# Kernel tuning notes

Hardware: AMD Instinct MI355X
Metric: run time of the kernel (lower is better)

## Reference

```python
import jax, jax.numpy as jnp
import numpy as np

B, D, H1, H2 = 512, 1024, 512, 128

def setup_inputs() -> dict:
    key = jax.random.key(0)
    ks = jax.random.split(key, 3)
    x = jax.random.normal(ks[0], (B, D), dtype=jnp.float32)
    W1 = jax.random.normal(ks[1], (H1, D), dtype=jnp.float32)
    W2 = jax.random.normal(ks[2], (H2, H1), dtype=jnp.float32)
    b1 = jnp.full((H1,), 0.1, dtype=jnp.float32)
    b2 = jnp.full((H2,), 0.1, dtype=jnp.float32)
    b3 = jnp.full((H1,), 0.1, dtype=jnp.float32)
    b_r = jnp.full((D,), 0.1, dtype=jnp.float32)
    return {"x": x, "W1": W1, "b1": b1, "W2": W2, "b2": b2, "b3": b3, "b_r": b_r}

def reference(x, W1, b1, W2, b2, b3, b_r):
    # encoder
    c1 = jax.nn.sigmoid(x @ W1.T + b1)          # [B, H1]
    c2 = jax.nn.sigmoid(c1 @ W2.T + b2)         # [B, H2]
    # decoder (tied weights)
    c3 = jax.nn.sigmoid(c2 @ W2 + b3)           # [B, H1]
    recover = c3 @ W1 + b_r                     # [B, D]
    # Jacobian of code w.r.t. x, batched (replaces per-sample diag+matmul loop):
    # Jac[b] = diag(c2'(b)) @ W2 @ diag(c1'(b)) @ W1
    s1p = c1 * (1.0 - c1)                       # [B, H1]
    s2p = c2 * (1.0 - c2)                       # [B, H2]
    M = s2p[:, :, None] * W2[None, :, :] * s1p[:, None, :]   # [B, H2, H1]
    Jac = jnp.einsum('bhk,kd->bhd', M, W1)      # [B, H2, D]
    return (recover, c2, Jac)
```

## Files before the change

kernel.cpp:

```cpp
#include <hip/hip_runtime.h>


typedef _Float16 f16x8 __attribute__((ext_vector_type(8)));
typedef _Float16 f16x4 __attribute__((ext_vector_type(4)));
typedef float    f32x4 __attribute__((ext_vector_type(4)));
typedef float    f32x2 __attribute__((ext_vector_type(2)));

__device__ __forceinline__ void gld_lds16(const _Float16* src, _Float16* dst_wave_uniform) {
    __builtin_amdgcn_global_load_lds((const __attribute__((address_space(1))) unsigned int*)src,
                                     (__attribute__((address_space(3))) unsigned int*)dst_wave_uniform,
                                     16, 0, 0);
}

__global__ __launch_bounds__(256) void prep_kernel(const float* __restrict__ W1,
                                                   const float* __restrict__ W2,
                                                   _Float16* __restrict__ W1T,
                                                   _Float16* __restrict__ W2h) {
    int bx = blockIdx.x;
    if (bx < 512) {
        __shared__ float tile[32][33];
        int dt = (bx & 31) * 32, kt = (bx >> 5) * 32;
        int tx = threadIdx.x & 31, ty = threadIdx.x >> 5;
        #pragma unroll
        for (int r = 0; r < 32; r += 8)
            tile[ty + r][tx] = W1[(kt + ty + r) * 1024 + dt + tx];
        __syncthreads();
        #pragma unroll
        for (int r = 0; r < 32; r += 8)
            W1T[(size_t)(dt + ty + r) * 512 + kt + tx] = (_Float16)tile[tx][ty + r];
    } else {
        int i = (bx - 512) * 1024 + threadIdx.x * 4;
        f32x4 v = *(const f32x4*)(W2 + i);
        f16x4 h;
        h.x = (_Float16)v.x; h.y = (_Float16)v.y; h.z = (_Float16)v.z; h.w = (_Float16)v.w;
        *(f16x4*)(W2h + i) = h;
    }
}

template <int EPI, bool TRANSB>
__global__ __launch_bounds__(256) void gemm_f32(const float* __restrict__ A,
                                                const float* __restrict__ Bm,
                                                const float* __restrict__ bias,
                                                float* __restrict__ C,
                                                float* __restrict__ Cd,
                                                _Float16* __restrict__ Ch,
                                                int M, int N, int K) {
    __shared__ __align__(16) float As[16][34];
    __shared__ __align__(16) float Bs[16][68];
    const int n0 = blockIdx.x * 64, m0 = blockIdx.y * 32;
    const int tid = threadIdx.x, tx = tid & 15, ty = tid >> 4;
    float acc[2][4] = {};

    for (int k0 = 0; k0 < K; k0 += 16) {
        #pragma unroll
        for (int r = 0; r < 2; ++r) {
            int m = (tid >> 4) + r * 16, k = tid & 15;
            As[k][m] = A[(size_t)(m0 + m) * K + k0 + k];
        }
        if (TRANSB) {
            #pragma unroll
            for (int r = 0; r < 4; ++r) {
                int n = (tid >> 4) + r * 16, k = tid & 15;
                Bs[k][n] = Bm[(size_t)(n0 + n) * K + k0 + k];
            }
        } else {
            #pragma unroll
            for (int r = 0; r < 4; ++r) {
                int k = (tid >> 6) + r * 4, n = tid & 63;
                Bs[k][n] = Bm[(size_t)(k0 + k) * N + n0 + n];
            }
        }
        __syncthreads();
        #pragma unroll
        for (int k = 0; k < 16; ++k) {
            f32x2 av = *(const f32x2*)&As[k][ty * 2];
            f32x4 bv = *(const f32x4*)&Bs[k][tx * 4];
            #pragma unroll
            for (int i = 0; i < 2; ++i)
                #pragma unroll
                for (int j = 0; j < 4; ++j)
                    acc[i][j] += av[i] * bv[j];
        }
        __syncthreads();
    }

    #pragma unroll
    for (int i = 0; i < 2; ++i) {
        int row = m0 + ty * 2 + i;
        #pragma unroll
        for (int j = 0; j < 4; ++j) {
            int col = n0 + tx * 4 + j;
            float z = acc[i][j] + bias[col];
            float s = 1.f / (1.f + __expf(-z));
            if constexpr (EPI == 1) {
                C[(size_t)row * N + col]  = s;
                Cd[(size_t)row * N + col] = s * (1.f - s);
            } else {
                Ch[(size_t)row * N + col] = (_Float16)s;
            }
        }
    }
}

__global__ __launch_bounds__(256) void build_A(const float* __restrict__ W2,
                                               const float* __restrict__ s1p,
                                               const float* __restrict__ s2p,
                                               _Float16* __restrict__ A_all) {
    const int b = blockIdx.x, tid = threadIdx.x;
    __shared__ float S1[512];
    __shared__ float S2[128];
    S1[tid]       = s1p[(size_t)b * 512 + tid];
    S1[tid + 256] = s1p[(size_t)b * 512 + tid + 256];
    if (tid < 128) S2[tid] = s2p[(size_t)b * 128 + tid];
    __syncthreads();
    _Float16* out = A_all + (size_t)b * 65536;
    #pragma unroll 4
    for (int i = 0; i < 32; ++i) {
        int c = tid + 256 * i;
        int h = c >> 6, k8 = (c & 63) * 8;
        f32x4 w0 = *(const f32x4*)(W2 + h * 512 + k8);
        f32x4 w1 = *(const f32x4*)(W2 + h * 512 + k8 + 4);
        float s2 = S2[h];
        f16x8 o;
        o[0] = (_Float16)(s2 * w0.x * S1[k8 + 0]);
        o[1] = (_Float16)(s2 * w0.y * S1[k8 + 1]);
        o[2] = (_Float16)(s2 * w0.z * S1[k8 + 2]);
        o[3] = (_Float16)(s2 * w0.w * S1[k8 + 3]);
        o[4] = (_Float16)(s2 * w1.x * S1[k8 + 4]);
        o[5] = (_Float16)(s2 * w1.y * S1[k8 + 5]);
        o[6] = (_Float16)(s2 * w1.z * S1[k8 + 6]);
        o[7] = (_Float16)(s2 * w1.w * S1[k8 + 7]);
        *(f16x8*)(out + h * 512 + k8) = o;
    }
}

template <bool HAS_BIAS>
__global__ __launch_bounds__(256) void mfma_bt(const _Float16* __restrict__ Abase,
                                               const _Float16* __restrict__ Bmat,
                                               const float* __restrict__ bias,
                                               float* __restrict__ OutBase,
                                               int K, int N,
                                               long aBatch, long oBatch) {
    __shared__ __align__(16) _Float16 Asl[128 * 64];
    __shared__ __align__(16) _Float16 Bsl[128 * 64];
    __shared__ float Bias[128];
    const _Float16* A = Abase + (size_t)blockIdx.z * aBatch;
    float* Out = OutBase + (size_t)blockIdx.z * oBatch;
    const int m0 = blockIdx.y * 128, n0 = blockIdx.x * 128;
    const int tid = threadIdx.x;
    const int lane = tid & 63, wave = tid >> 6;
    const int wm = (wave >> 1) * 64, wn = (wave & 1) * 64;
    const int l15 = lane & 15, q = lane >> 4;

    if (HAS_BIAS && tid < 128) Bias[tid] = bias[n0 + tid];

    f32x4 acc[4][4];
    #pragma unroll
    for (int i = 0; i < 4; ++i)
        #pragma unroll
        for (int j = 0; j < 4; ++j) acc[i][j] = (f32x4){0.f, 0.f, 0.f, 0.f};

    const int rbase = wave * 8 + (lane >> 3);
    const int kof   = (lane & 7) * 8;

    for (int k0 = 0; k0 < K; k0 += 64) {
        #pragma unroll
        for (int r = 0; r < 4; ++r) {
            gld_lds16(A    + (size_t)(m0 + r * 32 + rbase) * K + k0 + kof, Asl + (r * 32 + wave * 8) * 64);
            gld_lds16(Bmat + (size_t)(n0 + r * 32 + rbase) * K + k0 + kof, Bsl + (r * 32 + wave * 8) * 64);
        }
        __syncthreads();
        #pragma unroll
        for (int kk = 0; kk < 64; kk += 32) {
            f16x8 af[4], bf[4];
            #pragma unroll
            for (int i = 0; i < 4; ++i)
                af[i] = *(const f16x8*)(Asl + (wm + i * 16 + l15) * 64 + kk + q * 8);
            #pragma unroll
            for (int j = 0; j < 4; ++j)
                bf[j] = *(const f16x8*)(Bsl + (wn + j * 16 + l15) * 64 + kk + q * 8);
            #pragma unroll
            for (int i = 0; i < 4; ++i)
                #pragma unroll
                for (int j = 0; j < 4; ++j)
                    acc[i][j] = __builtin_amdgcn_mfma_f32_16x16x32_f16(af[i], bf[j], acc[i][j], 0, 0, 0);
        }
        __syncthreads();
    }

    #pragma unroll
    for (int i = 0; i < 4; ++i) {
        #pragma unroll
        for (int rg = 0; rg < 4; ++rg) {
            int m = m0 + wm + i * 16 + q * 4 + rg;
            #pragma unroll
            for (int j = 0; j < 4; ++j) {
                int dcol = wn + j * 16 + l15;
                float v = acc[i][j][rg];
                if (HAS_BIAS) v += Bias[dcol];
                Out[(size_t)m * N + n0 + dcol] = v;
            }
        }
    }
}

__global__ __launch_bounds__(256) void jac_kernel(const _Float16* __restrict__ W2h,
                                                  const _Float16* __restrict__ W1T,
                                                  const float* __restrict__ s1p,
                                                  const float* __restrict__ s2p,
                                                  float* __restrict__ Jac) {
    __shared__ __align__(16) _Float16 Asl[128 * 64];
    __shared__ __align__(16) _Float16 Bsl[128 * 64];
    __shared__ float Ssl[128];
    const int b  = blockIdx.y;
    const int n0 = blockIdx.x * 128;
    const int tid = threadIdx.x;
    const int lane = tid & 63, wave = tid >> 6;
    const int wm = (wave >> 1) * 64, wn = (wave & 1) * 64;
    const int l15 = lane & 15, q = lane >> 4;

    if (tid < 128) Ssl[tid] = s2p[b * 128 + tid];

    f32x4 acc[4][4];
    #pragma unroll
    for (int i = 0; i < 4; ++i)
        #pragma unroll
        for (int j = 0; j < 4; ++j) acc[i][j] = (f32x4){0.f, 0.f, 0.f, 0.f};

    const int ah  = tid >> 4;
    const int akq = (tid & 15) * 4;
    const int rbase = wave * 8 + (lane >> 3);
    const int kof   = (lane & 7) * 8;

    for (int k0 = 0; k0 < 512; k0 += 64) {
        f32x4 s4 = *(const f32x4*)(s1p + (size_t)b * 512 + k0 + akq);
        f16x4 s4h;
        s4h.x = (_Float16)s4.x; s4h.y = (_Float16)s4.y;
        s4h.z = (_Float16)s4.z; s4h.w = (_Float16)s4.w;
        #pragma unroll
        for (int r = 0; r < 8; ++r) {
            int h = ah + r * 16;
            f16x4 w4 = *(const f16x4*)(W2h + (size_t)h * 512 + k0 + akq);
            *(f16x4*)(Asl + h * 64 + akq) = w4 * s4h;
        }
        #pragma unroll
        for (int r = 0; r < 4; ++r)
            gld_lds16(W1T + (size_t)(n0 + r * 32 + rbase) * 512 + k0 + kof,
                      Bsl + (r * 32 + wave * 8) * 64);
        __syncthreads();

        #pragma unroll
        for (int kk = 0; kk < 64; kk += 32) {
            f16x8 af[4], bf[4];
            #pragma unroll
            for (int i = 0; i < 4; ++i)
                af[i] = *(const f16x8*)(Asl + (wm + i * 16 + l15) * 64 + kk + q * 8);
            #pragma unroll
            for (int j = 0; j < 4; ++j)
                bf[j] = *(const f16x8*)(Bsl + (wn + j * 16 + l15) * 64 + kk + q * 8);
            #pragma unroll
            for (int i = 0; i < 4; ++i)
                #pragma unroll
                for (int j = 0; j < 4; ++j)
                    acc[i][j] = __builtin_amdgcn_mfma_f32_16x16x32_f16(af[i], bf[j], acc[i][j], 0, 0, 0);
        }
        __syncthreads();
    }

    float* outb = Jac + (size_t)b * (128 * 1024);
    #pragma unroll
    for (int i = 0; i < 4; ++i) {
        #pragma unroll
        for (int rg = 0; rg < 4; ++rg) {
            int h = wm + i * 16 + q * 4 + rg;
            float s = Ssl[h];
            #pragma unroll
            for (int j = 0; j < 4; ++j) {
                int d = n0 + wn + j * 16 + l15;
                outb[(size_t)h * 1024 + d] = acc[i][j][rg] * s;
            }
        }
    }
}

extern "C" void kernel_launch(void* const* d_in, const int* in_sizes, int n_in,
                              void* d_out, int out_size, void* d_ws, size_t ws_size,
                              hipStream_t stream) {
    const float* x  = (const float*)d_in[0];
    const float* W1 = (const float*)d_in[1];
    const float* b1 = (const float*)d_in[2];
    const float* W2 = (const float*)d_in[3];
    const float* b2 = (const float*)d_in[4];
    const float* b3 = (const float*)d_in[5];
    const float* br = (const float*)d_in[6];

    float* out_rec = (float*)d_out;
    float* out_c2  = out_rec + 512 * 1024;
    float* out_jac = out_c2 + 512 * 128;

    char* ws = (char*)d_ws;
    _Float16* W1T   = (_Float16*)(ws);
    _Float16* W2h   = (_Float16*)(ws + 0x100000);
    float*    c1    = (float*)(ws + 0x120000);
    float*    s1p   = (float*)(ws + 0x220000);
    float*    s2p   = (float*)(ws + 0x320000);
    _Float16* c3h   = (_Float16*)(ws + 0x360000);
    _Float16* A_all = (_Float16*)(ws + 0x400000);
    const bool big_ws = ws_size >= (size_t)0x4400000;

    prep_kernel<<<576, 256, 0, stream>>>(W1, W2, W1T, W2h);
    gemm_f32<1, true ><<<dim3(8, 16), 256, 0, stream>>>(x,      W1, b1, c1,     s1p, nullptr, 512, 512, 1024);
    gemm_f32<1, true ><<<dim3(2, 16), 256, 0, stream>>>(c1,     W2, b2, out_c2, s2p, nullptr, 512, 128, 512);
    gemm_f32<2, false><<<dim3(8, 16), 256, 0, stream>>>(out_c2, W2, b3, nullptr, nullptr, c3h, 512, 512, 128);
    mfma_bt<true><<<dim3(8, 4, 1), 256, 0, stream>>>(c3h, W1T, br, out_rec, 512, 1024, 0, 0);
    if (big_ws) {
        build_A<<<512, 256, 0, stream>>>(W2, s1p, s2p, A_all);
        mfma_bt<false><<<dim3(8, 1, 512), 256, 0, stream>>>(A_all, W1T, nullptr, out_jac,
                                                            512, 1024, 65536, 131072);
    } else {
        jac_kernel<<<dim3(8, 512), 256, 0, stream>>>(W2h, W1T, s1p, s2p, out_jac);
    }
}
```

Baseline: 459.8 us.

## Fuse kernels, pipeline Jacobian GEMM with on-the-fly A build and double buffering

```diff
diff --git a/kernel.cpp b/kernel.cpp
--- a/kernel.cpp
+++ b/kernel.cpp
@@ -12,67 +12,70 @@
                                      16, 0, 0);
 }
 
-__global__ __launch_bounds__(256) void prep_kernel(const float* __restrict__ W1,
-                                                   const float* __restrict__ W2,
-                                                   _Float16* __restrict__ W1T,
-                                                   _Float16* __restrict__ W2h) {
-    int bx = blockIdx.x;
-    if (bx < 512) {
-        __shared__ float tile[32][33];
-        int dt = (bx & 31) * 32, kt = (bx >> 5) * 32;
-        int tx = threadIdx.x & 31, ty = threadIdx.x >> 5;
-        #pragma unroll
-        for (int r = 0; r < 32; r += 8)
-            tile[ty + r][tx] = W1[(kt + ty + r) * 1024 + dt + tx];
+__device__ __forceinline__ void prep_dev(int bx, const float* __restrict__ W1,
+                                         _Float16* __restrict__ W1T) {
+    __shared__ float tile[32][33];
+    int dt = (bx & 31) * 32, kt = (bx >> 5) * 32;
+    int tx = threadIdx.x & 31, ty = threadIdx.x >> 5;
+    #pragma unroll
+    for (int r = 0; r < 32; r += 8)
+        tile[ty + r][tx] = W1[(kt + ty + r) * 1024 + dt + tx];
+    __syncthreads();
+    #pragma unroll
+    for (int r = 0; r < 32; r += 8)
+        W1T[(size_t)(dt + ty + r) * 512 + kt + tx] = (_Float16)tile[tx][ty + r];
+}
+
+template <int EPI, bool TRANSB>
+__device__ void gemm_dev(const float* __restrict__ A, const float* __restrict__ Bm,
+                         const float* __restrict__ bias,
+                         float* __restrict__ C, float* __restrict__ Cd,
+                         _Float16* __restrict__ Ch,
+                         int M, int N, int K, int m0, int n0) {
+    __shared__ __align__(16) float As[32][34];
+    __shared__ __align__(16) float Bs[32][68];
+    const int tid = threadIdx.x, tx = tid & 15, ty = tid >> 4;
+    const int ka  = tid & 31, ma  = tid >> 5;
+    const int kbt = tid & 31, nbt = tid >> 5;
+    const int nbf = tid & 63, kbf = tid >> 6;
+    float acc[2][4] = {};
+    float rA[4], rB[8];
+
+    #pragma unroll
+    for (int r = 0; r < 4; ++r) rA[r] = A[(size_t)(m0 + ma + 8 * r) * K + ka];
+    if (TRANSB) {
+        #pragma unroll
+        for (int r = 0; r < 8; ++r) rB[r] = Bm[(size_t)(n0 + nbt + 8 * r) * K + kbt];
+    } else {
+        #pragma unroll
+        for (int r = 0; r < 8; ++r) rB[r] = Bm[(size_t)(kbf + 4 * r) * N + n0 + nbf];
+    }
+
+    for (int k0 = 0; k0 < K; k0 += 32) {
+        #pragma unroll
+        for (int r = 0; r < 4; ++r) As[ka][ma + 8 * r] = rA[r];
+        if (TRANSB) {
+            #pragma unroll
+            for (int r = 0; r < 8; ++r) Bs[kbt][nbt + 8 * r] = rB[r];
+        } else {
+            #pragma unroll
+            for (int r = 0; r < 8; ++r) Bs[kbf + 4 * r][nbf] = rB[r];
+        }
+        const int k1 = k0 + 32;
+        if (k1 < K) {
+            #pragma unroll
+            for (int r = 0; r < 4; ++r) rA[r] = A[(size_t)(m0 + ma + 8 * r) * K + k1 + ka];
+            if (TRANSB) {
+                #pragma unroll
+                for (int r = 0; r < 8; ++r) rB[r] = Bm[(size_t)(n0 + nbt + 8 * r) * K + k1 + kbt];
+            } else {
+                #pragma unroll
+                for (int r = 0; r < 8; ++r) rB[r] = Bm[(size_t)(k1 + kbf + 4 * r) * N + n0 + nbf];
+            }
+        }
         __syncthreads();
         #pragma unroll
-        for (int r = 0; r < 32; r += 8)
-            W1T[(size_t)(dt + ty + r) * 512 + kt + tx] = (_Float16)tile[tx][ty + r];
-    } else {
-        int i = (bx - 512) * 1024 + threadIdx.x * 4;
-        f32x4 v = *(const f32x4*)(W2 + i);
-        f16x4 h;
-        h.x = (_Float16)v.x; h.y = (_Float16)v.y; h.z = (_Float16)v.z; h.w = (_Float16)v.w;
-        *(f16x4*)(W2h + i) = h;
-    }
-}
-
-template <int EPI, bool TRANSB>
-__global__ __launch_bounds__(256) void gemm_f32(const float* __restrict__ A,
-                                                const float* __restrict__ Bm,
-                                                const float* __restrict__ bias,
-                                                float* __restrict__ C,
-                                                float* __restrict__ Cd,
-                                                _Float16* __restrict__ Ch,
-                                                int M, int N, int K) {
-    __shared__ __align__(16) float As[16][34];
-    __shared__ __align__(16) float Bs[16][68];
-    const int n0 = blockIdx.x * 64, m0 = blockIdx.y * 32;
-    const int tid = threadIdx.x, tx = tid & 15, ty = tid >> 4;
-    float acc[2][4] = {};
-
-    for (int k0 = 0; k0 < K; k0 += 16) {
-        #pragma unroll
-        for (int r = 0; r < 2; ++r) {
-            int m = (tid >> 4) + r * 16, k = tid & 15;
-            As[k][m] = A[(size_t)(m0 + m) * K + k0 + k];
-        }
-        if (TRANSB) {
-            #pragma unroll
-            for (int r = 0; r < 4; ++r) {
-                int n = (tid >> 4) + r * 16, k = tid & 15;
-                Bs[k][n] = Bm[(size_t)(n0 + n) * K + k0 + k];
-            }
-        } else {
-            #pragma unroll
-            for (int r = 0; r < 4; ++r) {
-                int k = (tid >> 6) + r * 4, n = tid & 63;
-                Bs[k][n] = Bm[(size_t)(k0 + k) * N + n0 + n];
-            }
-        }
-        __syncthreads();
-        #pragma unroll
-        for (int k = 0; k < 16; ++k) {
+        for (int k = 0; k < 32; ++k) {
             f32x2 av = *(const f32x2*)&As[k][ty * 2];
             f32x4 bv = *(const f32x4*)&Bs[k][tx * 4];
             #pragma unroll
@@ -102,57 +105,56 @@
     }
 }
 
-__global__ __launch_bounds__(256) void build_A(const float* __restrict__ W2,
-                                               const float* __restrict__ s1p,
-                                               const float* __restrict__ s2p,
-                                               _Float16* __restrict__ A_all) {
-    const int b = blockIdx.x, tid = threadIdx.x;
+__global__ __launch_bounds__(256) void fused_prep_gemm1(const float* __restrict__ x,
+                                                        const float* __restrict__ W1,
+                                                        const float* __restrict__ b1,
+                                                        _Float16* __restrict__ W1T,
+                                                        float* __restrict__ c1,
+                                                        float* __restrict__ s1p) {
+    int bx = blockIdx.x;
+    if (bx < 128) {
+        gemm_dev<1, true>(x, W1, b1, c1, s1p, nullptr, 512, 512, 1024,
+                          (bx >> 3) * 32, (bx & 7) * 64);
+    } else {
+        prep_dev(bx - 128, W1, W1T);
+    }
+}
+
+__global__ __launch_bounds__(256) void gemm2_kernel(const float* __restrict__ c1,
+                                                    const float* __restrict__ W2,
+                                                    const float* __restrict__ b2,
+                                                    float* __restrict__ out_c2,
+                                                    float* __restrict__ s2p) {
+    gemm_dev<1, true>(c1, W2, b2, out_c2, s2p, nullptr, 512, 128, 512,
+                      blockIdx.y * 32, blockIdx.x * 64);
+}
+
+__global__ __launch_bounds__(256) void gemm3_kernel(const float* __restrict__ out_c2,
+                                                    const float* __restrict__ W2,
+                                                    const float* __restrict__ b3,
+                                                    _Float16* __restrict__ c3h) {
+    gemm_dev<2, false>(out_c2, W2, b3, nullptr, nullptr, c3h, 512, 512, 128,
+                       (blockIdx.x >> 3) * 32, (blockIdx.x & 7) * 64);
+}
+
+__global__ __launch_bounds__(256, 2) void jacF_fused(const _Float16* __restrict__ c3h,
+                                                     const _Float16* __restrict__ W1T,
+                                                     const float* __restrict__ W2,
+                                                     const float* __restrict__ s1p,
+                                                     const float* __restrict__ s2p,
+                                                     const float* __restrict__ br,
+                                                     float* __restrict__ out_rec,
+                                                     float* __restrict__ out_jac) {
+    __shared__ __align__(16) _Float16 Asl[2][128 * 72];
+    __shared__ __align__(16) _Float16 Bsl[2][128 * 64];
     __shared__ float S1[512];
     __shared__ float S2[128];
-    S1[tid]       = s1p[(size_t)b * 512 + tid];
-    S1[tid + 256] = s1p[(size_t)b * 512 + tid + 256];
-    if (tid < 128) S2[tid] = s2p[(size_t)b * 128 + tid];
-    __syncthreads();
-    _Float16* out = A_all + (size_t)b * 65536;
-    #pragma unroll 4
-    for (int i = 0; i < 32; ++i) {
-        int c = tid + 256 * i;
-        int h = c >> 6, k8 = (c & 63) * 8;
-        f32x4 w0 = *(const f32x4*)(W2 + h * 512 + k8);
-        f32x4 w1 = *(const f32x4*)(W2 + h * 512 + k8 + 4);
-        float s2 = S2[h];
-        f16x8 o;
-        o[0] = (_Float16)(s2 * w0.x * S1[k8 + 0]);
-        o[1] = (_Float16)(s2 * w0.y * S1[k8 + 1]);
-        o[2] = (_Float16)(s2 * w0.z * S1[k8 + 2]);
-        o[3] = (_Float16)(s2 * w0.w * S1[k8 + 3]);
-        o[4] = (_Float16)(s2 * w1.x * S1[k8 + 4]);
-        o[5] = (_Float16)(s2 * w1.y * S1[k8 + 5]);
-        o[6] = (_Float16)(s2 * w1.z * S1[k8 + 6]);
-        o[7] = (_Float16)(s2 * w1.w * S1[k8 + 7]);
-        *(f16x8*)(out + h * 512 + k8) = o;
-    }
-}
-
-template <bool HAS_BIAS>
-__global__ __launch_bounds__(256) void mfma_bt(const _Float16* __restrict__ Abase,
-                                               const _Float16* __restrict__ Bmat,
-                                               const float* __restrict__ bias,
-                                               float* __restrict__ OutBase,
-                                               int K, int N,
-                                               long aBatch, long oBatch) {
-    __shared__ __align__(16) _Float16 Asl[128 * 64];
-    __shared__ __align__(16) _Float16 Bsl[128 * 64];
-    __shared__ float Bias[128];
-    const _Float16* A = Abase + (size_t)blockIdx.z * aBatch;
-    float* Out = OutBase + (size_t)blockIdx.z * oBatch;
-    const int m0 = blockIdx.y * 128, n0 = blockIdx.x * 128;
+
     const int tid = threadIdx.x;
     const int lane = tid & 63, wave = tid >> 6;
     const int wm = (wave >> 1) * 64, wn = (wave & 1) * 64;
     const int l15 = lane & 15, q = lane >> 4;
-
-    if (HAS_BIAS && tid < 128) Bias[tid] = bias[n0 + tid];
+    const int bid = blockIdx.x;
 
     f32x4 acc[4][4];
     #pragma unroll
@@ -160,124 +162,143 @@
         #pragma unroll
         for (int j = 0; j < 4; ++j) acc[i][j] = (f32x4){0.f, 0.f, 0.f, 0.f};
 
-    const int rbase = wave * 8 + (lane >> 3);
-    const int kof   = (lane & 7) * 8;
-
-    for (int k0 = 0; k0 < K; k0 += 64) {
-        #pragma unroll
-        for (int r = 0; r < 4; ++r) {
-            gld_lds16(A    + (size_t)(m0 + r * 32 + rbase) * K + k0 + kof, Asl + (r * 32 + wave * 8) * 64);
-            gld_lds16(Bmat + (size_t)(n0 + r * 32 + rbase) * K + k0 + kof, Bsl + (r * 32 + wave * 8) * 64);
-        }
-        __syncthreads();
+    if (bid < 32) {
+        const int m0 = (bid >> 3) * 128, n0 = (bid & 7) * 128;
+        if (tid < 128) S2[tid] = br[n0 + tid];
+        const int rbase = wave * 8 + (lane >> 3);
+        const int kof   = (lane & 7) * 8;
+        _Float16* As0 = &Asl[0][0];
+        _Float16* Bs0 = &Bsl[0][0];
+
+        for (int k0 = 0; k0 < 512; k0 += 64) {
+            #pragma unroll
+            for (int r = 0; r < 4; ++r) {
+                gld_lds16(c3h + (size_t)(m0 + r * 32 + rbase) * 512 + k0 + kof, As0 + (r * 32 + wave * 8) * 64);
+                gld_lds16(W1T + (size_t)(n0 + r * 32 + rbase) * 512 + k0 + kof, Bs0 + (r * 32 + wave * 8) * 64);
+            }
+            __syncthreads();
+            #pragma unroll
+            for (int kk = 0; kk < 64; kk += 32) {
+                f16x8 af[4], bf[4];
+                #pragma unroll
+                for (int i = 0; i < 4; ++i)
+                    af[i] = *(const f16x8*)(As0 + (wm + i * 16 + l15) * 64 + kk + q * 8);
+                #pragma unroll
+                for (int j = 0; j < 4; ++j)
+                    bf[j] = *(const f16x8*)(Bs0 + (wn + j * 16 + l15) * 64 + kk + q * 8);
+                #pragma unroll
+                for (int i = 0; i < 4; ++i)
+                    #pragma unroll
+                    for (int j = 0; j < 4; ++j)
+                        acc[i][j] = __builtin_amdgcn_mfma_f32_16x16x32_f16(af[i], bf[j], acc[i][j], 0, 0, 0);
+            }
+            __syncthreads();
+        }
+
+        #pragma unroll
+        for (int i = 0; i < 4; ++i) {
+            #pragma unroll
+            for (int rg = 0; rg < 4; ++rg) {
+                int m = m0 + wm + i * 16 + q * 4 + rg;
+                #pragma unroll
+                for (int j = 0; j < 4; ++j) {
+                    int dcol = wn + j * 16 + l15;
+                    __builtin_nontemporal_store(acc[i][j][rg] + S2[dcol],
+                                                out_rec + (size_t)m * 1024 + n0 + dcol);
+                }
+            }
+        }
+        return;
+    }
+
+    const int jid = bid - 32;
+    const int w = (jid & 7) * 512 + (jid >> 3);
+    const int b = w >> 3, n0 = (w & 7) * 128;
+
+    S1[tid]       = s1p[(size_t)b * 512 + tid];
+    S1[tid + 256] = s1p[(size_t)b * 512 + 256 + tid];
+    if (tid < 128) S2[tid] = s2p[(size_t)b * 128 + tid];
+
+    const int arow = tid >> 1;
+    const int akh  = (tid & 1) * 32;
+    const float* W2r = W2 + arow * 512;
+    const int srow = wave * 8 + (lane >> 3);
+    const int skof = ((lane & 7) ^ (lane >> 3)) * 8;
+    const _Float16* Bbase = W1T + (size_t)n0 * 512;
+    const int swz = (l15 & 7) * 8;
+
+    f32x4 wv[8];
+
+    auto ALOAD = [&](int t) {
+        const int kb = t * 64 + akh;
+        #pragma unroll
+        for (int u = 0; u < 8; ++u) wv[u] = *(const f32x4*)(W2r + kb + u * 4);
+    };
+    auto BSTAGE = [&](int t) {
+        const int buf = t & 1, kb = t * 64;
+        #pragma unroll
+        for (int r = 0; r < 4; ++r)
+            gld_lds16(Bbase + (size_t)(r * 32 + srow) * 512 + kb + skof,
+                      &Bsl[buf][(r * 32 + wave * 8) * 64]);
+    };
+    auto ADSW = [&](int t) {
+        const int buf = t & 1, kb = t * 64 + akh;
+        #pragma unroll
+        for (int j8 = 0; j8 < 4; ++j8) {
+            f16x8 av;
+            #pragma unroll
+            for (int e = 0; e < 8; ++e) {
+                int xx = j8 * 8 + e;
+                av[e] = (_Float16)(wv[xx >> 2][xx & 3] * S1[kb + xx]);
+            }
+            *(f16x8*)(&Asl[buf][arow * 72 + akh + j8 * 8]) = av;
+        }
+    };
+
+    ALOAD(0);
+    BSTAGE(0);
+    __syncthreads();
+    ADSW(0);
+    ALOAD(1);
+    BSTAGE(1);
+    __syncthreads();
+
+    #pragma unroll 1
+    for (int t = 0; t < 8; ++t) {
+        const int buf = t & 1;
+        const _Float16* As = &Asl[buf][0];
+        const _Float16* Bs = &Bsl[buf][0];
         #pragma unroll
         for (int kk = 0; kk < 64; kk += 32) {
             f16x8 af[4], bf[4];
             #pragma unroll
             for (int i = 0; i < 4; ++i)
-                af[i] = *(const f16x8*)(Asl + (wm + i * 16 + l15) * 64 + kk + q * 8);
+                af[i] = *(const f16x8*)(As + (wm + i * 16 + l15) * 72 + kk + q * 8);
             #pragma unroll
             for (int j = 0; j < 4; ++j)
-                bf[j] = *(const f16x8*)(Bsl + (wn + j * 16 + l15) * 64 + kk + q * 8);
+                bf[j] = *(const f16x8*)(Bs + (wn + j * 16 + l15) * 64 + ((kk + q * 8) ^ swz));
             #pragma unroll
             for (int i = 0; i < 4; ++i)
                 #pragma unroll
                 for (int j = 0; j < 4; ++j)
                     acc[i][j] = __builtin_amdgcn_mfma_f32_16x16x32_f16(af[i], bf[j], acc[i][j], 0, 0, 0);
         }
+        if (t < 7) ADSW(t + 1);
         __syncthreads();
-    }
-
-    #pragma unroll
-    for (int i = 0; i < 4; ++i) {
-        #pragma unroll
-        for (int rg = 0; rg < 4; ++rg) {
-            int m = m0 + wm + i * 16 + q * 4 + rg;
-            #pragma unroll
-            for (int j = 0; j < 4; ++j) {
-                int dcol = wn + j * 16 + l15;
-                float v = acc[i][j][rg];
-                if (HAS_BIAS) v += Bias[dcol];
-                Out[(size_t)m * N + n0 + dcol] = v;
-            }
-        }
-    }
-}
-
-__global__ __launch_bounds__(256) void jac_kernel(const _Float16* __restrict__ W2h,
-                                                  const _Float16* __restrict__ W1T,
-                                                  const float* __restrict__ s1p,
-                                                  const float* __restrict__ s2p,
-                                                  float* __restrict__ Jac) {
-    __shared__ __align__(16) _Float16 Asl[128 * 64];
-    __shared__ __align__(16) _Float16 Bsl[128 * 64];
-    __shared__ float Ssl[128];
-    const int b  = blockIdx.y;
-    const int n0 = blockIdx.x * 128;
-    const int tid = threadIdx.x;
-    const int lane = tid & 63, wave = tid >> 6;
-    const int wm = (wave >> 1) * 64, wn = (wave & 1) * 64;
-    const int l15 = lane & 15, q = lane >> 4;
-
-    if (tid < 128) Ssl[tid] = s2p[b * 128 + tid];
-
-    f32x4 acc[4][4];
-    #pragma unroll
-    for (int i = 0; i < 4; ++i)
-        #pragma unroll
-        for (int j = 0; j < 4; ++j) acc[i][j] = (f32x4){0.f, 0.f, 0.f, 0.f};
-
-    const int ah  = tid >> 4;
-    const int akq = (tid & 15) * 4;
-    const int rbase = wave * 8 + (lane >> 3);
-    const int kof   = (lane & 7) * 8;
-
-    for (int k0 = 0; k0 < 512; k0 += 64) {
-        f32x4 s4 = *(const f32x4*)(s1p + (size_t)b * 512 + k0 + akq);
-        f16x4 s4h;
-        s4h.x = (_Float16)s4.x; s4h.y = (_Float16)s4.y;
-        s4h.z = (_Float16)s4.z; s4h.w = (_Float16)s4.w;
-        #pragma unroll
-        for (int r = 0; r < 8; ++r) {
-            int h = ah + r * 16;
-            f16x4 w4 = *(const f16x4*)(W2h + (size_t)h * 512 + k0 + akq);
-            *(f16x4*)(Asl + h * 64 + akq) = w4 * s4h;
-        }
-        #pragma unroll
-        for (int r = 0; r < 4; ++r)
-            gld_lds16(W1T + (size_t)(n0 + r * 32 + rbase) * 512 + k0 + kof,
-                      Bsl + (r * 32 + wave * 8) * 64);
-        __syncthreads();
-
-        #pragma unroll
-        for (int kk = 0; kk < 64; kk += 32) {
-            f16x8 af[4], bf[4];
-            #pragma unroll
-            for (int i = 0; i < 4; ++i)
-                af[i] = *(const f16x8*)(Asl + (wm + i * 16 + l15) * 64 + kk + q * 8);
-            #pragma unroll
-            for (int j = 0; j < 4; ++j)
-                bf[j] = *(const f16x8*)(Bsl + (wn + j * 16 + l15) * 64 + kk + q * 8);
-            #pragma unroll
-            for (int i = 0; i < 4; ++i)
-                #pragma unroll
-                for (int j = 0; j < 4; ++j)
-                    acc[i][j] = __builtin_amdgcn_mfma_f32_16x16x32_f16(af[i], bf[j], acc[i][j], 0, 0, 0);
-        }
-        __syncthreads();
-    }
-
-    float* outb = Jac + (size_t)b * (128 * 1024);
+        if (t < 6) { ALOAD(t + 2); BSTAGE(t + 2); }
+    }
+
+    float* outb = out_jac + (size_t)b * (128 * 1024);
     #pragma unroll
     for (int i = 0; i < 4; ++i) {
         #pragma unroll
         for (int rg = 0; rg < 4; ++rg) {
             int h = wm + i * 16 + q * 4 + rg;
-            float s = Ssl[h];
+            float s = S2[h];
             #pragma unroll
             for (int j = 0; j < 4; ++j) {
                 int d = n0 + wn + j * 16 + l15;
-                outb[(size_t)h * 1024 + d] = acc[i][j][rg] * s;
+                __builtin_nontemporal_store(acc[i][j][rg] * s, outb + (size_t)h * 1024 + d);
             }
         }
     }
@@ -299,25 +320,14 @@
     float* out_jac = out_c2 + 512 * 128;
 
     char* ws = (char*)d_ws;
-    _Float16* W1T   = (_Float16*)(ws);
-    _Float16* W2h   = (_Float16*)(ws + 0x100000);
-    float*    c1    = (float*)(ws + 0x120000);
-    float*    s1p   = (float*)(ws + 0x220000);
-    float*    s2p   = (float*)(ws + 0x320000);
-    _Float16* c3h   = (_Float16*)(ws + 0x360000);
-    _Float16* A_all = (_Float16*)(ws + 0x400000);
-    const bool big_ws = ws_size >= (size_t)0x4400000;
-
-    prep_kernel<<<576, 256, 0, stream>>>(W1, W2, W1T, W2h);
-    gemm_f32<1, true ><<<dim3(8, 16), 256, 0, stream>>>(x,      W1, b1, c1,     s1p, nullptr, 512, 512, 1024);
-    gemm_f32<1, true ><<<dim3(2, 16), 256, 0, stream>>>(c1,     W2, b2, out_c2, s2p, nullptr, 512, 128, 512);
-    gemm_f32<2, false><<<dim3(8, 16), 256, 0, stream>>>(out_c2, W2, b3, nullptr, nullptr, c3h, 512, 512, 128);
-    mfma_bt<true><<<dim3(8, 4, 1), 256, 0, stream>>>(c3h, W1T, br, out_rec, 512, 1024, 0, 0);
-    if (big_ws) {
-        build_A<<<512, 256, 0, stream>>>(W2, s1p, s2p, A_all);
-        mfma_bt<false><<<dim3(8, 1, 512), 256, 0, stream>>>(A_all, W1T, nullptr, out_jac,
-                                                            512, 1024, 65536, 131072);
-    } else {
-        jac_kernel<<<dim3(8, 512), 256, 0, stream>>>(W2h, W1T, s1p, s2p, out_jac);
-    }
-}
+    _Float16* W1T = (_Float16*)(ws);
+    float*    c1  = (float*)(ws + 0x100000);
+    float*    s1p = (float*)(ws + 0x200000);
+    float*    s2p = (float*)(ws + 0x300000);
+    _Float16* c3h = (_Float16*)(ws + 0x340000);
+
+    fused_prep_gemm1<<<640, 256, 0, stream>>>(x, W1, b1, W1T, c1, s1p);
+    gemm2_kernel<<<dim3(2, 16), 256, 0, stream>>>(c1, W2, b2, out_c2, s2p);
+    gemm3_kernel<<<128, 256, 0, stream>>>(out_c2, W2, b3, c3h);
+    jacF_fused<<<4128, 256, 0, stream>>>(c3h, W1T, W2, s1p, s2p, br, out_rec, out_jac);
+}
```

Measured after the change: 492.8 us. 7.2% more time.
